# Kernel optimization log

Hardware: AMD Instinct MI355X
Metric: run time of the kernel (lower is better)

The kernel has to match this reference:

```python
import jax, jax.numpy as jnp
import numpy as np

# --- constants hardcoded in the torch Model ---
VIEWS = [45.0, 90.0, 135.0, 225.0, 270.0, 315.0]
DIST, ELEV = 1.5, 15.0          # look_at_view_transform(1.5, 15, views)
S = 128                          # image_size
K = 5                            # points_per_pixel
RADIUS = 0.01                    # NDC radius
R2 = RADIUS * RADIUS
ZNEAR, ZFAR = 0.01, 100.0        # FoVOrthographicCameras defaults
BIG = 1e9                        # depth sentinel for non-covering points


def look_at_RT():
    """PyTorch3D look_at_view_transform: world->view is X @ R + T."""
    azim = jnp.deg2rad(jnp.asarray(VIEWS, jnp.float32))
    elev = jnp.deg2rad(jnp.float32(ELEV))
    # camera centers [V,3]
    C = DIST * jnp.stack([jnp.cos(elev) * jnp.sin(azim),
                          jnp.sin(elev) * jnp.ones_like(azim),
                          jnp.cos(elev) * jnp.cos(azim)], axis=-1)
    up = jnp.broadcast_to(jnp.asarray([0.0, 1.0, 0.0], jnp.float32), C.shape)
    z = -C / jnp.linalg.norm(C, axis=-1, keepdims=True)          # at(=0) - eye
    x = jnp.cross(up, z)
    x = x / jnp.linalg.norm(x, axis=-1, keepdims=True)
    y = jnp.cross(z, x)
    y = y / jnp.linalg.norm(y, axis=-1, keepdims=True)
    R = jnp.stack([x, y, z], axis=-1)                            # [V,3,3] cols = axes
    T = -jnp.einsum('vj,vji->vi', C, R)                          # camera -> origin
    return R, T


def render_view(R, T, pts, feats):
    """PointsRasterizer + AlphaCompositor for one FoVOrthographic camera.
    pts [N,3] world, feats [N,3]. Returns image [S,S,3]."""
    pv = pts @ R + T                                             # [N,3] view space
    px, py, pz = pv[:, 0], pv[:, 1], pv[:, 2]
    # orthographic NDC with max_x=max_y=1, min=-1, scale=1 -> ndc_xy == view_xy
    valid = (pz > ZNEAR) & (pz < ZFAR)
    # PyTorch3D pixel centers: PixToNdc(i,S)=(2i+1-S)/S, with x and y flipped
    pix = (2.0 * jnp.arange(S, dtype=pts.dtype) + 1.0 - S) / S
    xf = pix[::-1]                                               # +X is left
    yf = pix[::-1]                                               # +Y is up (row 0 = top)
    dx = xf[None, :, None] - px[None, None, :]                   # [1,S,N]
    dy = yf[:, None, None] - py[None, None, :]                   # [S,1,N]
    d2 = dx * dx + dy * dy                                       # [S,S,N]
    hit = (d2 < R2) & valid[None, None, :]
    score = jnp.where(hit, pz[None, None, :], BIG)               # sort hits by depth
    neg_z, idx = jax.lax.top_k(-score, K)                        # K nearest, [S,S,K]
    ok = (-neg_z) < 0.5 * BIG
    d2k = jnp.take_along_axis(d2, idx, axis=-1)                  # [S,S,K]
    w = jnp.where(ok, 1.0 - d2k / R2, 0.0)                       # alphas in (0,1]
    fk = feats[idx]                                              # [S,S,K,3]
    # front-to-back alpha compositing: sum_k w_k * prod_{j<k}(1-w_j) * f_k
    trans = jnp.cumprod(1.0 - w, axis=-1)
    prefix = jnp.concatenate([jnp.ones_like(w[..., :1]), trans[..., :-1]], axis=-1)
    img = jnp.einsum('hwk,hwkc->hwc', w * prefix, fk)            # background = 0
    return img


def setup_inputs() -> dict:
    key = jax.random.key(0)
    k1, k2 = jax.random.split(key)
    pcd = 0.3 * jax.random.normal(k1, (4096, 3), dtype=jnp.float32)  # inside NDC window
    init_colors = jnp.zeros((4096,), dtype=jnp.float32)
    displace = jax.random.normal(k2, (4096,), dtype=jnp.float32)
    return {"pcd": pcd, "init_colors": init_colors, "displace": displace}


def reference(pcd, init_colors, displace):
    colors_ = jax.nn.sigmoid(init_colors + displace)             # [N]
    feats = jnp.broadcast_to(colors_[:, None], (colors_.shape[0], 3))  # repeat to 3 ch
    R, T = look_at_RT()
    images = jax.lax.map(lambda rt: render_view(rt[0], rt[1], pcd, feats), (R, T))
    return images, colors_                                       # [6,128,128,3], [4096]
```

## Files before the change

kernel.cpp:

```cpp
#include <hip/hip_runtime.h>
#include <hip/hip_bf16.h>
#include <math.h>

#define NPTS 4096
#define SDIM 128
#define NV 6
#define KTOP 5
#define IMG_ELEMS (NV * SDIM * SDIM * 3)

#define R2F 1e-4f
#define RMARG 0.0102f

#define RBW 32
#define RBH 16
#define NBLK (NV * 32)
#define NCX 8
#define NCY 4
#define NCELL 32
#define CAPS 128

struct CamParams { float R[NV][9]; float T[NV][3]; };

__device__ __forceinline__ float sigmoidf_fast(float x) {
  return __fdividef(1.0f, 1.0f + __expf(-x));
}

__device__ __forceinline__ void process_cand(
    float4 P, float xf, float yf,
    float zk[KTOP], float wk[KTOP], float ck[KTOP]) {
  float dx = xf - P.x;
  float dy = yf - P.y;
  float d2 = dx * dx + dy * dy;
  if (d2 < R2F) {
    float wgt = 1.0f - d2 / R2F;
    float z = P.z;
    if (z < zk[KTOP - 1]) {
      zk[KTOP - 1] = z; wk[KTOP - 1] = wgt; ck[KTOP - 1] = P.w;
#pragma unroll
      for (int k = KTOP - 1; k > 0; k--) {
        if (zk[k] < zk[k - 1]) {
          float tz = zk[k]; zk[k] = zk[k - 1]; zk[k - 1] = tz;
          float tw = wk[k]; wk[k] = wk[k - 1]; wk[k - 1] = tw;
          float tc = ck[k]; ck[k] = ck[k - 1]; ck[k - 1] = tc;
        }
      }
    }
  }
}

__global__ __launch_bounds__(512) void fused_render_kernel(
    const float4* __restrict__ pcd4,
    const float4* __restrict__ add0_4,
    const float4* __restrict__ add1_4,
    float* __restrict__ out,
    float4* __restrict__ out_colors4,
    CamParams cams) {
  int b = blockIdx.x;
  int v = b >> 5;
  int t = b & 31;
  int ty = t >> 2, tx = t & 3;
  int tid = threadIdx.x;
  int w0 = tx * RBW, h0 = ty * RBH;
  int row = tid >> 5, col = tid & 31;
  int h = h0 + row;
  int w = w0 + col;
  float xf = (float)(127 - 2 * w) * (1.0f / 128.0f);
  float yf = (float)(127 - 2 * h) * (1.0f / 128.0f);

  float xhi = (float)(127 - 2 * w0) * (1.0f / 128.0f) + RMARG;
  float xlo = (float)(127 - 2 * (w0 + RBW - 1)) * (1.0f / 128.0f) - RMARG;
  float yhi = (float)(127 - 2 * h0) * (1.0f / 128.0f) + RMARG;
  float ylo = (float)(127 - 2 * (h0 + RBH - 1)) * (1.0f / 128.0f) - RMARG;

  __shared__ float4 cand[NCELL][CAPS + 1];
  __shared__ int cnts[NCELL];
  if (tid < NCELL) cnts[tid] = 0;
  __syncthreads();

  const float* Rp = cams.R[v];
  const float* Tp = cams.T[v];
  float R0 = Rp[0], R1 = Rp[1], R2 = Rp[2];
  float R3 = Rp[3], R4 = Rp[4], R5 = Rp[5];
  float R6 = Rp[6], R7 = Rp[7], R8 = Rp[8];
  float T0 = Tp[0], T1 = Tp[1], T2 = Tp[2];

  float4 A[2][3], C0[2], C1[2];
#pragma unroll
  for (int k = 0; k < 2; k++) {
    int g = k * 512 + tid;
    A[k][0] = pcd4[3 * g + 0];
    A[k][1] = pcd4[3 * g + 1];
    A[k][2] = pcd4[3 * g + 2];
    C0[k] = add0_4[g];
    C1[k] = add1_4[g];
  }

  if (b < 2) {
    int g = b * 512 + tid;
    float4 s;
    s.x = sigmoidf_fast(C0[b].x + C1[b].x);
    s.y = sigmoidf_fast(C0[b].y + C1[b].y);
    s.z = sigmoidf_fast(C0[b].z + C1[b].z);
    s.w = sigmoidf_fast(C0[b].w + C1[b].w);
    out_colors4[g] = s;
  }

#pragma unroll
  for (int k = 0; k < 2; k++) {
    float f[12] = {A[k][0].x, A[k][0].y, A[k][0].z, A[k][0].w,
                   A[k][1].x, A[k][1].y, A[k][1].z, A[k][1].w,
                   A[k][2].x, A[k][2].y, A[k][2].z, A[k][2].w};
    float sc[4] = {sigmoidf_fast(C0[k].x + C1[k].x),
                   sigmoidf_fast(C0[k].y + C1[k].y),
                   sigmoidf_fast(C0[k].z + C1[k].z),
                   sigmoidf_fast(C0[k].w + C1[k].w)};
#pragma unroll
    for (int j = 0; j < 4; j++) {
      float p0 = f[3 * j + 0], p1 = f[3 * j + 1], p2 = f[3 * j + 2];
      float px = p0 * R0 + p1 * R3 + p2 * R6 + T0;
      float py = p0 * R1 + p1 * R4 + p2 * R7 + T1;
      float pz = p0 * R2 + p1 * R5 + p2 * R8 + T2;
      if (pz > 0.01f && pz < 100.0f &&
          px > xlo && px < xhi && py > ylo && py < yhi) {
        float lwlo = (127.0f - 128.0f * (px + RMARG)) * 0.5f - (float)w0;
        float lwhi = (127.0f - 128.0f * (px - RMARG)) * 0.5f - (float)w0;
        float lhlo = (127.0f - 128.0f * (py + RMARG)) * 0.5f - (float)h0;
        float lhhi = (127.0f - 128.0f * (py - RMARG)) * 0.5f - (float)h0;
        int cxlo = (int)fmaxf(0.0f, floorf(lwlo * 0.25f));
        int cxhi = (int)fminf((float)(NCX - 1), floorf(lwhi * 0.25f));
        int cylo = (int)fmaxf(0.0f, floorf(lhlo * 0.25f));
        int cyhi = (int)fminf((float)(NCY - 1), floorf(lhhi * 0.25f));
        float4 payload = make_float4(px, py, pz, sc[j]);
        for (int cy = cylo; cy <= cyhi; cy++)
          for (int cx = cxlo; cx <= cxhi; cx++) {
            int li = cy * NCX + cx;
            int idx = atomicAdd(&cnts[li], 1);
            if (idx < CAPS) cand[li][idx] = payload;
          }
      }
    }
  }
  __syncthreads();

  int li = (row >> 2) * NCX + (col >> 2);
  int n = cnts[li];
  if (n > CAPS) n = CAPS;
  const float4* list = cand[li];

  float zk[KTOP], wk[KTOP], ck[KTOP];
#pragma unroll
  for (int k = 0; k < KTOP; k++) { zk[k] = 1e30f; wk[k] = 0.0f; ck[k] = 0.0f; }

  int j = 0;
  for (; j + 8 <= n; j += 8) {
    float4 P0 = list[j + 0], P1 = list[j + 1], P2 = list[j + 2], P3 = list[j + 3];
    float4 P4 = list[j + 4], P5 = list[j + 5], P6 = list[j + 6], P7 = list[j + 7];
    process_cand(P0, xf, yf, zk, wk, ck);
    process_cand(P1, xf, yf, zk, wk, ck);
    process_cand(P2, xf, yf, zk, wk, ck);
    process_cand(P3, xf, yf, zk, wk, ck);
    process_cand(P4, xf, yf, zk, wk, ck);
    process_cand(P5, xf, yf, zk, wk, ck);
    process_cand(P6, xf, yf, zk, wk, ck);
    process_cand(P7, xf, yf, zk, wk, ck);
  }
  for (; j < n; j++) {
    float4 P = list[j];
    process_cand(P, xf, yf, zk, wk, ck);
  }

  float acc = 0.0f, pre = 1.0f;
#pragma unroll
  for (int k = 0; k < KTOP; k++) {
    acc += wk[k] * pre * ck[k];
    pre *= (1.0f - wk[k]);
  }

  int base = v * (SDIM * SDIM * 3) + (h * SDIM + w) * 3;
  out[base + 0] = acc;
  out[base + 1] = acc;
  out[base + 2] = acc;
}

static void compute_cams(CamParams* cp) {
  const double views[NV] = {45.0, 90.0, 135.0, 225.0, 270.0, 315.0};
  const double deg = M_PI / 180.0;
  const double elev = 15.0 * deg;
  const double dist = 1.5;
  for (int v = 0; v < NV; v++) {
    double az = views[v] * deg;
    double C[3] = {dist * cos(elev) * sin(az), dist * sin(elev),
                   dist * cos(elev) * cos(az)};
    double n = sqrt(C[0] * C[0] + C[1] * C[1] + C[2] * C[2]);
    double z[3] = {-C[0] / n, -C[1] / n, -C[2] / n};
    double up[3] = {0.0, 1.0, 0.0};
    double x[3] = {up[1] * z[2] - up[2] * z[1],
                   up[2] * z[0] - up[0] * z[2],
                   up[0] * z[1] - up[1] * z[0]};
    double nx = sqrt(x[0] * x[0] + x[1] * x[1] + x[2] * x[2]);
    x[0] /= nx; x[1] /= nx; x[2] /= nx;
    double y[3] = {z[1] * x[2] - z[2] * x[1],
                   z[2] * x[0] - z[0] * x[2],
                   z[0] * x[1] - z[1] * x[0]};
    double ny = sqrt(y[0] * y[0] + y[1] * y[1] + y[2] * y[2]);
    y[0] /= ny; y[1] /= ny; y[2] /= ny;
    double Rm[3][3];
    for (int j = 0; j < 3; j++) { Rm[j][0] = x[j]; Rm[j][1] = y[j]; Rm[j][2] = z[j]; }
    for (int j = 0; j < 3; j++)
      for (int i = 0; i < 3; i++)
        cp->R[v][j * 3 + i] = (float)Rm[j][i];
    for (int i = 0; i < 3; i++)
      cp->T[v][i] = (float)(-(C[0] * Rm[0][i] + C[1] * Rm[1][i] + C[2] * Rm[2][i]));
  }
}

extern "C" void kernel_launch(void* const* d_in, const int* in_sizes, int n_in,
                              void* d_out, int out_size, void* d_ws, size_t ws_size,
                              hipStream_t stream) {
  CamParams cp;
  compute_cams(&cp);

  const float* pcd = nullptr;
  const float* adds[2] = {nullptr, nullptr};
  int na = 0;
  for (int i = 0; i < n_in; i++) {
    if (in_sizes[i] == 3 * NPTS) pcd = (const float*)d_in[i];
    else if (na < 2) adds[na++] = (const float*)d_in[i];
  }
  if (!pcd || na < 2) { pcd = (const float*)d_in[0];
                        adds[0] = (const float*)d_in[1];
                        adds[1] = (const float*)d_in[2]; }

  float* out = (float*)d_out;
  float4* out_colors4 = (float4*)(out + IMG_ELEMS);

  fused_render_kernel<<<NBLK, 512, 0, stream>>>(
      (const float4*)pcd, (const float4*)adds[0], (const float4*)adds[1],
      out, out_colors4, cp);
}
```

Measured before the change: 75.21 us.

## Split each pixel's candidate scan across two threads and merge top-K results

Raster tiles shrink from 32x16 to 16x16 pixels, doubling the block count to 384 while keeping 512 threads per block. Two threads now share each pixel: each scans every other candidate in the cell list, and the two sorted top-5 lists are merged through shared memory before compositing. This aims to shorten the serial per-pixel candidate loop and fill more compute units. In exchange, every block still loads and projects all 4096 points, so total projection work doubles. The merge adds two barriers, and its data-dependent indexing into register arrays may be placed in scratch memory.

```diff
diff --git a/kernel.cpp b/kernel.cpp
--- a/kernel.cpp
+++ b/kernel.cpp
@@ -11,12 +11,11 @@
 #define R2F 1e-4f
 #define RMARG 0.0102f
 
-#define RBW 32
-#define RBH 16
-#define NBLK (NV * 32)
-#define NCX 8
+#define RB 16
+#define NBLK (NV * 64)
+#define NCX 4
 #define NCY 4
-#define NCELL 32
+#define NCELL 16
 #define CAPS 128
 
 struct CamParams { float R[NV][9]; float T[NV][3]; };
@@ -56,21 +55,23 @@
     float4* __restrict__ out_colors4,
     CamParams cams) {
   int b = blockIdx.x;
-  int v = b >> 5;
-  int t = b & 31;
-  int ty = t >> 2, tx = t & 3;
+  int v = b >> 6;
+  int t = b & 63;
+  int ty = t >> 3, tx = t & 7;
   int tid = threadIdx.x;
-  int w0 = tx * RBW, h0 = ty * RBH;
-  int row = tid >> 5, col = tid & 31;
+  int half = tid >> 8;
+  int p = tid & 255;
+  int row = p >> 4, col = p & 15;
+  int w0 = tx * RB, h0 = ty * RB;
   int h = h0 + row;
   int w = w0 + col;
   float xf = (float)(127 - 2 * w) * (1.0f / 128.0f);
   float yf = (float)(127 - 2 * h) * (1.0f / 128.0f);
 
   float xhi = (float)(127 - 2 * w0) * (1.0f / 128.0f) + RMARG;
-  float xlo = (float)(127 - 2 * (w0 + RBW - 1)) * (1.0f / 128.0f) - RMARG;
+  float xlo = (float)(127 - 2 * (w0 + RB - 1)) * (1.0f / 128.0f) - RMARG;
   float yhi = (float)(127 - 2 * h0) * (1.0f / 128.0f) + RMARG;
-  float ylo = (float)(127 - 2 * (h0 + RBH - 1)) * (1.0f / 128.0f) - RMARG;
+  float ylo = (float)(127 - 2 * (h0 + RB - 1)) * (1.0f / 128.0f) - RMARG;
 
   __shared__ float4 cand[NCELL][CAPS + 1];
   __shared__ int cnts[NCELL];
@@ -151,35 +152,55 @@
 #pragma unroll
   for (int k = 0; k < KTOP; k++) { zk[k] = 1e30f; wk[k] = 0.0f; ck[k] = 0.0f; }
 
-  int j = 0;
-  for (; j + 8 <= n; j += 8) {
-    float4 P0 = list[j + 0], P1 = list[j + 1], P2 = list[j + 2], P3 = list[j + 3];
-    float4 P4 = list[j + 4], P5 = list[j + 5], P6 = list[j + 6], P7 = list[j + 7];
+  int j = half;
+  for (; j + 6 < n; j += 8) {
+    float4 P0 = list[j + 0], P1 = list[j + 2], P2 = list[j + 4], P3 = list[j + 6];
     process_cand(P0, xf, yf, zk, wk, ck);
     process_cand(P1, xf, yf, zk, wk, ck);
     process_cand(P2, xf, yf, zk, wk, ck);
     process_cand(P3, xf, yf, zk, wk, ck);
-    process_cand(P4, xf, yf, zk, wk, ck);
-    process_cand(P5, xf, yf, zk, wk, ck);
-    process_cand(P6, xf, yf, zk, wk, ck);
-    process_cand(P7, xf, yf, zk, wk, ck);
-  }
-  for (; j < n; j++) {
+  }
+  for (; j < n; j += 2) {
     float4 P = list[j];
     process_cand(P, xf, yf, zk, wk, ck);
   }
 
-  float acc = 0.0f, pre = 1.0f;
-#pragma unroll
-  for (int k = 0; k < KTOP; k++) {
-    acc += wk[k] * pre * ck[k];
-    pre *= (1.0f - wk[k]);
-  }
-
-  int base = v * (SDIM * SDIM * 3) + (h * SDIM + w) * 3;
-  out[base + 0] = acc;
-  out[base + 1] = acc;
-  out[base + 2] = acc;
+  __syncthreads();
+  float4* mbuf = &cand[0][0];
+  if (half) {
+#pragma unroll
+    for (int k = 0; k < KTOP; k++)
+      mbuf[p * KTOP + k] = make_float4(zk[k], wk[k], ck[k], 0.0f);
+  }
+  __syncthreads();
+  if (!half) {
+    float oz[KTOP], ow[KTOP], oc[KTOP];
+#pragma unroll
+    for (int k = 0; k < KTOP; k++) {
+      float4 q = mbuf[p * KTOP + k];
+      oz[k] = q.x; ow[k] = q.y; oc[k] = q.z;
+    }
+    float mw[KTOP], mc[KTOP];
+    int a = 0, bq = 0;
+#pragma unroll
+    for (int k = 0; k < KTOP; k++) {
+      bool takeA = zk[a] <= oz[bq];
+      mw[k] = takeA ? wk[a] : ow[bq];
+      mc[k] = takeA ? ck[a] : oc[bq];
+      a += takeA ? 1 : 0;
+      bq += takeA ? 0 : 1;
+    }
+    float acc = 0.0f, pre = 1.0f;
+#pragma unroll
+    for (int k = 0; k < KTOP; k++) {
+      acc += mw[k] * pre * mc[k];
+      pre *= (1.0f - mw[k]);
+    }
+    int base = v * (SDIM * SDIM * 3) + (h * SDIM + w) * 3;
+    out[base + 0] = acc;
+    out[base + 1] = acc;
+    out[base + 2] = acc;
+  }
 }
 
 static void compute_cams(CamParams* cp) {
```

Result: slower. 79.45 us (+5.6%).
